# Optimization experiments

Hardware: AMD Instinct MI355X
Metric: run time of the kernel (lower is better)

## Reference

```python
import jax, jax.numpy as jnp
import numpy as np

N_ITER = 2
M = 0.0
AFF_SOFTMAX = 1.0
BIG = 1e16  # finite sentinel for invalid neighbors (CUDA kernel uses inf)


def _ssn(x, s):
    B, C, H, W = x.shape
    nh, nw = H // s, W // s
    S = nh * nw
    N = H * W
    # append_grid: concat (row, col) coordinate channels scaled by M/stoken
    ii, jj = jnp.meshgrid(jnp.arange(H), jnp.arange(W), indexing='ij')
    grid = jnp.stack([ii, jj], 0).astype(x.dtype) * (M / s)  # (2,H,W)
    xg = jnp.concatenate([x, jnp.broadcast_to(grid[None], (B, 2, H, W))], 1)
    C2 = C + 2
    # adaptive_avg_pool2d with exact divisibility == block mean
    cent = xg.reshape(B, C2, nh, s, nw, s).mean(axis=(3, 5)).reshape(B, C2, S)
    # nearest-neighbor init label map (exact divisibility => i//s)
    ly = jnp.broadcast_to((jnp.arange(H) // s)[:, None], (H, W)).reshape(-1)
    lx = jnp.broadcast_to((jnp.arange(W) // s)[None, :], (H, W)).reshape(-1)
    dy = jnp.repeat(jnp.arange(-1, 2), 3)  # 9-neighborhood offsets
    dx = jnp.tile(jnp.arange(-1, 2), 3)
    ny = ly[None, :] + dy[:, None]  # (9,N)
    nx = lx[None, :] + dx[:, None]
    valid = (ny >= 0) & (ny < nh) & (nx >= 0) & (nx < nw)
    nidx = jnp.clip(ny, 0, nh - 1) * nw + jnp.clip(nx, 0, nw - 1)  # (9,N)
    pix = jnp.arange(N)
    bidx = jnp.arange(B)[:, None, None]
    px = xg.reshape(B, C2, N)
    abs_aff = None
    for k in range(N_ITER):
        cg = cent[:, :, nidx]                              # (B,C2,9,N) gather
        dist = ((px[:, :, None, :] - cg) ** 2).sum(1)      # (B,9,N)
        dist = jnp.where(valid[None], dist, BIG)
        aff = jax.nn.softmax(-AFF_SOFTMAX * dist, axis=1)  # softmax over 9 nbrs
        aff = jnp.where(valid[None], aff, 0.0)
        # sparse_coo_tensor(...).to_dense() == scatter-add into (B,S,N)
        abs_aff = jnp.zeros((B, S, N), x.dtype).at[bidx, nidx[None], pix].add(aff)
        if k < N_ITER - 1:
            num = jnp.einsum('bsn,bcn->bcs', abs_aff, px)  # weighted bmm
            den = abs_aff.sum(2)[:, None] + 1e-16
            cent = num / den
    return abs_aff, S


def setup_inputs() -> dict:
    key = jax.random.key(0)
    x = jax.random.normal(key, (4, 32, 256, 256), dtype=jnp.float32)
    return {"x": x, "stoken_size": 16}


def reference(x, stoken_size):
    return _ssn(x, int(stoken_size))
```

## Files before the change

### kernel.cpp

```cpp
#include <hip/hip_runtime.h>
#include <hip/hip_fp16.h>
#include <hip/hip_cooperative_groups.h>

namespace cg = cooperative_groups;

#define B_  4
#define C_  32
#define W_  256
#define N_  65536
#define NH_ 16
#define S_  256
#define PADP 260
#define PADH 260
#define PSTR 304

typedef float vf4 __attribute__((ext_vector_type(4)));
typedef _Float16 h4 __attribute__((ext_vector_type(4)));

__device__ __forceinline__ float wave_sum(float v) {
    v += __shfl_down(v, 32);
    v += __shfl_down(v, 16);
    v += __shfl_down(v, 8);
    v += __shfl_down(v, 4);
    v += __shfl_down(v, 2);
    v += __shfl_down(v, 1);
    return v;
}

__device__ __forceinline__ void st4(float* p, float a, float b, float c, float d) {
    vf4 v = {a, b, c, d};
    *(vf4*)p = v;
}

__device__ __forceinline__ void zero_linear(float* out, int blk, int t,
                                            int i0, int i1) {
    vf4* p = (vf4*)out;
    const size_t base = (size_t)blk * 256 + t;
    const vf4 z = {0.f, 0.f, 0.f, 0.f};
    #pragma unroll 8
    for (int i = i0; i < i1; ++i)
        p[base + (size_t)i * 262144] = z;
}

__device__ __forceinline__ void stage_tile(const float* __restrict__ x,
                                           int b, int sy, int sx, int t,
                                           float (*xsh)[PADP]) {
    const float* base = x + (size_t)b * C_ * N_ + (sy * 16) * W_ + sx * 16;
    #pragma unroll
    for (int i = 0; i < 8; ++i) {
        const int idx = i * 256 + t;
        const int c = idx >> 6, p4 = idx & 63;
        const float4 v = *(const float4*)(base + (size_t)c * N_ + (p4 >> 2) * W_ + (p4 & 3) * 4);
        *(float4*)&xsh[c][p4 * 4] = v;
    }
}

__device__ __forceinline__ void compute_aff(const float xv[C_], const float (*cl)[C_],
                                            int sy, int sx, float aff[9]) {
    float dist[9];
    #pragma unroll
    for (int k = 0; k < 9; ++k) {
        const int ny = sy + k / 3 - 1, nx = sx + k % 3 - 1;
        const bool valid = (ny >= 0) & (ny < NH_) & (nx >= 0) & (nx < NH_);
        float d = 0.f;
        #pragma unroll
        for (int c4 = 0; c4 < C_ / 4; ++c4) {
            const float4 cv = *(const float4*)&cl[k][c4 * 4];
            const float d0 = xv[c4 * 4 + 0] - cv.x;
            const float d1 = xv[c4 * 4 + 1] - cv.y;
            const float d2 = xv[c4 * 4 + 2] - cv.z;
            const float d3 = xv[c4 * 4 + 3] - cv.w;
            d += d0 * d0 + d1 * d1 + d2 * d2 + d3 * d3;
        }
        dist[k] = valid ? d : 1e30f;
    }
    float mind = dist[0];
    #pragma unroll
    for (int k = 1; k < 9; ++k) mind = fminf(mind, dist[k]);
    float sum = 0.f;
    #pragma unroll
    for (int k = 0; k < 9; ++k) {
        const float e = (dist[k] < 1e29f) ? __expf(mind - dist[k]) : 0.f;
        aff[k] = e;
        sum += e;
    }
    const float inv = 1.f / sum;
    #pragma unroll
    for (int k = 0; k < 9; ++k) aff[k] *= inv;
}

__device__ __forceinline__ float gather_cent1(const float* __restrict__ part,
                                              int b, int ny, int nx, int c) {
    float num = 0.f, den = 0.f;
    #pragma unroll
    for (int k2 = 0; k2 < 9; ++k2) {
        const int syp = ny - (k2 / 3 - 1), sxp = nx - (k2 % 3 - 1);
        if ((syp >= 0) & (syp < NH_) & (sxp >= 0) & (sxp < NH_)) {
            const size_t base = (size_t)(b * S_ + syp * NH_ + sxp) * PSTR;
            num += part[base + k2 * 32 + c];
            den += part[base + 288 + k2];
        }
    }
    return num / (den + 1e-16f);
}

__global__ __launch_bounds__(256, 4) void k_fused(const float* __restrict__ x,
                                                  float* __restrict__ cent0,
                                                  float* __restrict__ part,
                                                  float* __restrict__ out) {
    const int blk = blockIdx.x;
    const int b = blk >> 8, s = blk & 255;
    const int sy = s >> 4, sx = s & 15;
    const int t = threadIdx.x;
    const int w = t >> 6, lane = t & 63;
    __shared__ float cl[9][C_];
    __shared__ float xsh[C_][PADP];
    __shared__ _Float16 affs[9][PADH];
    __shared__ float lden[4][9];

    stage_tile(x, b, sy, sx, t, xsh);
    zero_linear(out, blk, t, 0, 32);
    __syncthreads();
    #pragma unroll
    for (int i = 0; i < 8; ++i) {
        const int c = i * 4 + w;
        const float4 v = *(const float4*)&xsh[c][lane * 4];
        const float sm = wave_sum(v.x + v.y + v.z + v.w);
        if (lane == 0) cent0[(size_t)blk * C_ + c] = sm * (1.0f / 256.0f);
    }
    cg::this_grid().sync();

    {
        const int k = t >> 5, c = t & 31;
        const int ny = sy + k / 3 - 1, nx = sx + k % 3 - 1;
        const bool valid = (ny >= 0) & (ny < NH_) & (nx >= 0) & (nx < NH_);
        cl[k][c] = valid ? cent0[(size_t)(b * S_ + ny * NH_ + nx) * C_ + c] : 0.f;
    }
    if (t < 32) {
        const int ny = sy + 1, nx = sx + 1;
        const bool valid = (ny < NH_) & (nx < NH_);
        cl[8][t] = valid ? cent0[(size_t)(b * S_ + ny * NH_ + nx) * C_ + t] : 0.f;
    }
    zero_linear(out, blk, t, 32, 64);
    __syncthreads();
    float xv[C_];
    #pragma unroll
    for (int c = 0; c < C_; ++c) xv[c] = xsh[c][t];
    float aff[9];
    compute_aff(xv, cl, sy, sx, aff);
    #pragma unroll
    for (int k = 0; k < 9; ++k) {
        affs[k][t] = (_Float16)aff[k];
        const float v = wave_sum(aff[k]);
        if (lane == 0) lden[w][k] = v;
    }
    __syncthreads();
    {
        const int k = t >> 5, c = t & 31;
        float acc = 0.f;
        #pragma unroll 4
        for (int p = 0; p < 256; p += 4) {
            const h4 a = *(const h4*)&affs[k][p];
            const float4 xc = *(const float4*)&xsh[c][p];
            acc += (float)a.x * xc.x + (float)a.y * xc.y +
                   (float)a.z * xc.z + (float)a.w * xc.w;
        }
        part[(size_t)blk * PSTR + t] = acc;
    }
    if (t < 32) {
        float acc = 0.f;
        #pragma unroll 4
        for (int p = 0; p < 256; p += 4) {
            const h4 a = *(const h4*)&affs[8][p];
            const float4 xc = *(const float4*)&xsh[t][p];
            acc += (float)a.x * xc.x + (float)a.y * xc.y +
                   (float)a.z * xc.z + (float)a.w * xc.w;
        }
        part[(size_t)blk * PSTR + 256 + t] = acc;
    }
    if (t < 9)
        part[(size_t)blk * PSTR + 288 + t] =
            lden[0][t] + lden[1][t] + lden[2][t] + lden[3][t];
    cg::this_grid().sync();

    {
        const int k = t >> 5, c = t & 31;
        const int ny = sy + k / 3 - 1, nx = sx + k % 3 - 1;
        const bool valid = (ny >= 0) & (ny < NH_) & (nx >= 0) & (nx < NH_);
        cl[k][c] = valid ? gather_cent1(part, b, ny, nx, c) : 0.f;
    }
    if (t < 32) {
        const int ny = sy + 1, nx = sx + 1;
        const bool valid = (ny < NH_) & (nx < NH_);
        cl[8][t] = valid ? gather_cent1(part, b, ny, nx, t) : 0.f;
    }
    __syncthreads();
    #pragma unroll
    for (int c = 0; c < C_; ++c) xv[c] = xsh[c][t];
    compute_aff(xv, cl, sy, sx, aff);
    #pragma unroll
    for (int k = 0; k < 9; ++k) affs[k][t] = (_Float16)aff[k];
    __syncthreads();
    #pragma unroll
    for (int i = 0; i < 3; ++i) {
        const int idx = i * 256 + t;
        if (idx < 576) {
            const int k = idx >> 6, j4 = idx & 63;
            const int ny = sy + k / 3 - 1, nx = sx + k % 3 - 1;
            if ((ny >= 0) & (ny < NH_) & (nx >= 0) & (nx < NH_)) {
                const h4 a = *(const h4*)&affs[k][j4 * 4];
                const int gq = (sy * 16 + (j4 >> 2)) * 64 + sx * 4 + (j4 & 3);
                float* dst = out + (((size_t)(b * S_ + ny * NH_ + nx) << 16) + gq * 4);
                st4(dst, (float)a.x, (float)a.y, (float)a.z, (float)a.w);
            }
        }
    }
    if ((blk | t) == 0) out[(size_t)B_ * S_ * N_] = 256.0f;
}

__global__ __launch_bounds__(256) void k_zero(float* __restrict__ out) {
    const size_t tid = (size_t)blockIdx.x * 256 + threadIdx.x;
    vf4* p = (vf4*)out;
    const vf4 z = {0.f, 0.f, 0.f, 0.f};
    #pragma unroll 4
    for (int i = 0; i < 32; ++i)
        p[tid + (size_t)i * 524288] = z;
}

__global__ __launch_bounds__(256) void k_cent0(const float* __restrict__ x,
                                               float* __restrict__ cent0) {
    const int blk = blockIdx.x;
    const int b = blk >> 8, s = blk & 255;
    const int sy = s >> 4, sx = s & 15;
    const int t = threadIdx.x;
    const int w = t >> 6, lane = t & 63;
    const float* base = x + (size_t)b * C_ * N_ + (sy * 16) * W_ + sx * 16;
    #pragma unroll
    for (int i = 0; i < 8; ++i) {
        const int c = i * 4 + w;
        const float4 v = *(const float4*)(base + (size_t)c * N_ + (lane >> 2) * W_ + (lane & 3) * 4);
        const float sm = wave_sum(v.x + v.y + v.z + v.w);
        if (lane == 0) cent0[(size_t)blk * C_ + c] = sm * (1.0f / 256.0f);
    }
}

__global__ __launch_bounds__(256, 4) void k_part(const float* __restrict__ x,
                                                 const float* __restrict__ cent0,
                                                 float* __restrict__ part) {
    const int blk = blockIdx.x;
    const int b = blk >> 8, s = blk & 255;
    const int sy = s >> 4, sx = s & 15;
    const int t = threadIdx.x;
    const int w = t >> 6, lane = t & 63;
    __shared__ float cl[9][C_];
    __shared__ float xsh[C_][PADP];
    __shared__ _Float16 affs[9][PADH];
    __shared__ float lden[4][9];
    {
        const int k = t >> 5, c = t & 31;
        const int ny = sy + k / 3 - 1, nx = sx + k % 3 - 1;
        const bool valid = (ny >= 0) & (ny < NH_) & (nx >= 0) & (nx < NH_);
        cl[k][c] = valid ? cent0[(size_t)(b * S_ + ny * NH_ + nx) * C_ + c] : 0.f;
    }
    if (t < 32) {
        const int ny = sy + 1, nx = sx + 1;
        const bool valid = (ny < NH_) & (nx < NH_);
        cl[8][t] = valid ? cent0[(size_t)(b * S_ + ny * NH_ + nx) * C_ + t] : 0.f;
    }
    stage_tile(x, b, sy, sx, t, xsh);
    __syncthreads();
    float xv[C_];
    #pragma unroll
    for (int c = 0; c < C_; ++c) xv[c] = xsh[c][t];
    float aff[9];
    compute_aff(xv, cl, sy, sx, aff);
    #pragma unroll
    for (int k = 0; k < 9; ++k) {
        affs[k][t] = (_Float16)aff[k];
        const float v = wave_sum(aff[k]);
        if (lane == 0) lden[w][k] = v;
    }
    __syncthreads();
    {
        const int k = t >> 5, c = t & 31;
        float acc = 0.f;
        #pragma unroll 4
        for (int p = 0; p < 256; p += 4) {
            const h4 a = *(const h4*)&affs[k][p];
            const float4 xc = *(const float4*)&xsh[c][p];
            acc += (float)a.x * xc.x + (float)a.y * xc.y +
                   (float)a.z * xc.z + (float)a.w * xc.w;
        }
        part[(size_t)blk * PSTR + t] = acc;
    }
    if (t < 32) {
        float acc = 0.f;
        #pragma unroll 4
        for (int p = 0; p < 256; p += 4) {
            const h4 a = *(const h4*)&affs[8][p];
            const float4 xc = *(const float4*)&xsh[t][p];
            acc += (float)a.x * xc.x + (float)a.y * xc.y +
                   (float)a.z * xc.z + (float)a.w * xc.w;
        }
        part[(size_t)blk * PSTR + 256 + t] = acc;
    }
    if (t < 9)
        part[(size_t)blk * PSTR + 288 + t] =
            lden[0][t] + lden[1][t] + lden[2][t] + lden[3][t];
}

__global__ __launch_bounds__(256, 4) void k_aff9(const float* __restrict__ x,
                                                 const float* __restrict__ part,
                                                 float* __restrict__ out) {
    const int blk = blockIdx.x;
    const int b = blk >> 8, s = blk & 255;
    const int sy = s >> 4, sx = s & 15;
    const int t = threadIdx.x;
    __shared__ float cl[9][C_];
    __shared__ float xsh[C_][PADP];
    __shared__ _Float16 affs[9][PADH];
    {
        const int k = t >> 5, c = t & 31;
        const int ny = sy + k / 3 - 1, nx = sx + k % 3 - 1;
        const bool valid = (ny >= 0) & (ny < NH_) & (nx >= 0) & (nx < NH_);
        cl[k][c] = valid ? gather_cent1(part, b, ny, nx, c) : 0.f;
    }
    if (t < 32) {
        const int ny = sy + 1, nx = sx + 1;
        const bool valid = (ny < NH_) & (nx < NH_);
        cl[8][t] = valid ? gather_cent1(part, b, ny, nx, t) : 0.f;
    }
    stage_tile(x, b, sy, sx, t, xsh);
    __syncthreads();
    float xv[C_];
    #pragma unroll
    for (int c = 0; c < C_; ++c) xv[c] = xsh[c][t];
    float aff[9];
    compute_aff(xv, cl, sy, sx, aff);
    #pragma unroll
    for (int k = 0; k < 9; ++k) affs[k][t] = (_Float16)aff[k];
    __syncthreads();
    #pragma unroll
    for (int i = 0; i < 3; ++i) {
        const int idx = i * 256 + t;
        if (idx < 576) {
            const int k = idx >> 6, j4 = idx & 63;
            const int ny = sy + k / 3 - 1, nx = sx + k % 3 - 1;
            if ((ny >= 0) & (ny < NH_) & (nx >= 0) & (nx < NH_)) {
                const h4 a = *(const h4*)&affs[k][j4 * 4];
                const int gq = (sy * 16 + (j4 >> 2)) * 64 + sx * 4 + (j4 & 3);
                float* dst = out + (((size_t)(b * S_ + ny * NH_ + nx) << 16) + gq * 4);
                st4(dst, (float)a.x, (float)a.y, (float)a.z, (float)a.w);
            }
        }
    }
    if ((blk | t) == 0) out[(size_t)B_ * S_ * N_] = 256.0f;
}

extern "C" void kernel_launch(void* const* d_in, const int* in_sizes, int n_in,
                              void* d_out, int out_size, void* d_ws, size_t ws_size,
                              hipStream_t stream) {
    const float* x = (const float*)d_in[0];
    float* ws = (float*)d_ws;
    float* cent0 = ws;
    float* part  = ws + 32768;
    float* out   = (float*)d_out;

    static int coop_ok = -1;
    if (coop_ok < 0) {
        int nb = 0;
        hipError_t e = hipOccupancyMaxActiveBlocksPerMultiprocessor(&nb, k_fused, 256, 0);
        coop_ok = (e == hipSuccess && nb >= 4) ? 1 : 0;
    }

    if (coop_ok == 1) {
        void* args[] = {(void*)&x, (void*)&cent0, (void*)&part, (void*)&out};
        hipError_t e = hipLaunchCooperativeKernel((void*)k_fused, dim3(B_ * S_),
                                                  dim3(256), args, 0, stream);
        if (e == hipSuccess) return;
        coop_ok = 0;
    }

    hipLaunchKernelGGL(k_zero,  dim3(2048),    dim3(256), 0, stream, out);
    hipLaunchKernelGGL(k_cent0, dim3(B_ * S_), dim3(256), 0, stream, x, cent0);
    hipLaunchKernelGGL(k_part,  dim3(B_ * S_), dim3(256), 0, stream, x, cent0, part);
    hipLaunchKernelGGL(k_aff9,  dim3(B_ * S_), dim3(256), 0, stream, x, part, out);
}
```

Measured before the change: 348.7 us.

## Write compact affinities to workspace, then emit dense output in one streaming pass

New measurement: 346.2 us. Within noise of the previous version (-0.7%).

```diff
diff --git a/kernel.cpp b/kernel.cpp
--- a/kernel.cpp
+++ b/kernel.cpp
@@ -27,21 +27,6 @@
     return v;
 }
 
-__device__ __forceinline__ void st4(float* p, float a, float b, float c, float d) {
-    vf4 v = {a, b, c, d};
-    *(vf4*)p = v;
-}
-
-__device__ __forceinline__ void zero_linear(float* out, int blk, int t,
-                                            int i0, int i1) {
-    vf4* p = (vf4*)out;
-    const size_t base = (size_t)blk * 256 + t;
-    const vf4 z = {0.f, 0.f, 0.f, 0.f};
-    #pragma unroll 8
-    for (int i = i0; i < i1; ++i)
-        p[base + (size_t)i * 262144] = z;
-}
-
 __device__ __forceinline__ void stage_tile(const float* __restrict__ x,
                                            int b, int sy, int sx, int t,
                                            float (*xsh)[PADP]) {
@@ -104,10 +89,36 @@
     return num / (den + 1e-16f);
 }
 
-__global__ __launch_bounds__(256, 4) void k_fused(const float* __restrict__ x,
-                                                  float* __restrict__ cent0,
-                                                  float* __restrict__ part,
-                                                  float* __restrict__ out) {
+__global__ __launch_bounds__(256) void k_write(const float* __restrict__ vals,
+                                               float* __restrict__ out) {
+    const size_t tid = (size_t)blockIdx.x * 256 + threadIdx.x;
+    vf4* po = (vf4*)out;
+    #pragma unroll 4
+    for (int i = 0; i < 32; ++i) {
+        const size_t q = tid + (size_t)i * 524288;
+        const int b   = (int)(q >> 22);
+        const int r   = (int)(q & 4194303);
+        const int sp  = r >> 14;
+        const int n4  = r & 16383;
+        const int py  = n4 >> 6, px4 = n4 & 63;
+        const int syp = sp >> 4,  sxp = sp & 15;
+        const int ty  = py >> 4,  tx  = px4 >> 2;
+        vf4 v = {0.f, 0.f, 0.f, 0.f};
+        if (((unsigned)(ty - syp + 1) <= 2u) & ((unsigned)(tx - sxp + 1) <= 2u)) {
+            const int ssrc = ty * 16 + tx;
+            const int kp   = (syp - ty + 1) * 3 + (sxp - tx + 1);
+            const int pl   = (py & 15) * 16 + (px4 & 3) * 4;
+            v = *(const vf4*)&vals[(((size_t)(b * S_ + ssrc) * 9) + kp) * 256 + pl];
+        }
+        po[q] = v;
+    }
+    if (tid == 0) out[(size_t)B_ * S_ * N_] = 256.0f;
+}
+
+__global__ __launch_bounds__(256, 4) void k_compute(const float* __restrict__ x,
+                                                    float* __restrict__ cent0,
+                                                    float* __restrict__ part,
+                                                    float* __restrict__ vals) {
     const int blk = blockIdx.x;
     const int b = blk >> 8, s = blk & 255;
     const int sy = s >> 4, sx = s & 15;
@@ -119,7 +130,6 @@
     __shared__ float lden[4][9];
 
     stage_tile(x, b, sy, sx, t, xsh);
-    zero_linear(out, blk, t, 0, 32);
     __syncthreads();
     #pragma unroll
     for (int i = 0; i < 8; ++i) {
@@ -141,7 +151,6 @@
         const bool valid = (ny < NH_) & (nx < NH_);
         cl[8][t] = valid ? cent0[(size_t)(b * S_ + ny * NH_ + nx) * C_ + t] : 0.f;
     }
-    zero_linear(out, blk, t, 32, 64);
     __syncthreads();
     float xv[C_];
     #pragma unroll
@@ -199,32 +208,8 @@
     for (int c = 0; c < C_; ++c) xv[c] = xsh[c][t];
     compute_aff(xv, cl, sy, sx, aff);
     #pragma unroll
-    for (int k = 0; k < 9; ++k) affs[k][t] = (_Float16)aff[k];
-    __syncthreads();
-    #pragma unroll
-    for (int i = 0; i < 3; ++i) {
-        const int idx = i * 256 + t;
-        if (idx < 576) {
-            const int k = idx >> 6, j4 = idx & 63;
-            const int ny = sy + k / 3 - 1, nx = sx + k % 3 - 1;
-            if ((ny >= 0) & (ny < NH_) & (nx >= 0) & (nx < NH_)) {
-                const h4 a = *(const h4*)&affs[k][j4 * 4];
-                const int gq = (sy * 16 + (j4 >> 2)) * 64 + sx * 4 + (j4 & 3);
-                float* dst = out + (((size_t)(b * S_ + ny * NH_ + nx) << 16) + gq * 4);
-                st4(dst, (float)a.x, (float)a.y, (float)a.z, (float)a.w);
-            }
-        }
-    }
-    if ((blk | t) == 0) out[(size_t)B_ * S_ * N_] = 256.0f;
-}
-
-__global__ __launch_bounds__(256) void k_zero(float* __restrict__ out) {
-    const size_t tid = (size_t)blockIdx.x * 256 + threadIdx.x;
-    vf4* p = (vf4*)out;
-    const vf4 z = {0.f, 0.f, 0.f, 0.f};
-    #pragma unroll 4
-    for (int i = 0; i < 32; ++i)
-        p[tid + (size_t)i * 524288] = z;
+    for (int k = 0; k < 9; ++k)
+        vals[(((size_t)blk * 9) + k) * 256 + t] = aff[k];
 }
 
 __global__ __launch_bounds__(256) void k_cent0(const float* __restrict__ x,
@@ -309,16 +294,15 @@
             lden[0][t] + lden[1][t] + lden[2][t] + lden[3][t];
 }
 
-__global__ __launch_bounds__(256, 4) void k_aff9(const float* __restrict__ x,
-                                                 const float* __restrict__ part,
-                                                 float* __restrict__ out) {
+__global__ __launch_bounds__(256, 4) void k_aff9v(const float* __restrict__ x,
+                                                  const float* __restrict__ part,
+                                                  float* __restrict__ vals) {
     const int blk = blockIdx.x;
     const int b = blk >> 8, s = blk & 255;
     const int sy = s >> 4, sx = s & 15;
     const int t = threadIdx.x;
     __shared__ float cl[9][C_];
     __shared__ float xsh[C_][PADP];
-    __shared__ _Float16 affs[9][PADH];
     {
         const int k = t >> 5, c = t & 31;
         const int ny = sy + k / 3 - 1, nx = sx + k % 3 - 1;
@@ -338,23 +322,8 @@
     float aff[9];
     compute_aff(xv, cl, sy, sx, aff);
     #pragma unroll
-    for (int k = 0; k < 9; ++k) affs[k][t] = (_Float16)aff[k];
-    __syncthreads();
-    #pragma unroll
-    for (int i = 0; i < 3; ++i) {
-        const int idx = i * 256 + t;
-        if (idx < 576) {
-            const int k = idx >> 6, j4 = idx & 63;
-            const int ny = sy + k / 3 - 1, nx = sx + k % 3 - 1;
-            if ((ny >= 0) & (ny < NH_) & (nx >= 0) & (nx < NH_)) {
-                const h4 a = *(const h4*)&affs[k][j4 * 4];
-                const int gq = (sy * 16 + (j4 >> 2)) * 64 + sx * 4 + (j4 & 3);
-                float* dst = out + (((size_t)(b * S_ + ny * NH_ + nx) << 16) + gq * 4);
-                st4(dst, (float)a.x, (float)a.y, (float)a.z, (float)a.w);
-            }
-        }
-    }
-    if ((blk | t) == 0) out[(size_t)B_ * S_ * N_] = 256.0f;
+    for (int k = 0; k < 9; ++k)
+        vals[(((size_t)blk * 9) + k) * 256 + t] = aff[k];
 }
 
 extern "C" void kernel_launch(void* const* d_in, const int* in_sizes, int n_in,
@@ -364,25 +333,29 @@
     float* ws = (float*)d_ws;
     float* cent0 = ws;
     float* part  = ws + 32768;
+    float* vals  = ws + 32768 + 311296;
     float* out   = (float*)d_out;
 
     static int coop_ok = -1;
     if (coop_ok < 0) {
         int nb = 0;
-        hipError_t e = hipOccupancyMaxActiveBlocksPerMultiprocessor(&nb, k_fused, 256, 0);
+        hipError_t e = hipOccupancyMaxActiveBlocksPerMultiprocessor(&nb, k_compute, 256, 0);
         coop_ok = (e == hipSuccess && nb >= 4) ? 1 : 0;
     }
 
+    bool launched = false;
     if (coop_ok == 1) {
-        void* args[] = {(void*)&x, (void*)&cent0, (void*)&part, (void*)&out};
-        hipError_t e = hipLaunchCooperativeKernel((void*)k_fused, dim3(B_ * S_),
+        void* args[] = {(void*)&x, (void*)&cent0, (void*)&part, (void*)&vals};
+        hipError_t e = hipLaunchCooperativeKernel((void*)k_compute, dim3(B_ * S_),
                                                   dim3(256), args, 0, stream);
-        if (e == hipSuccess) return;
-        coop_ok = 0;
-    }
-
-    hipLaunchKernelGGL(k_zero,  dim3(2048),    dim3(256), 0, stream, out);
-    hipLaunchKernelGGL(k_cent0, dim3(B_ * S_), dim3(256), 0, stream, x, cent0);
-    hipLaunchKernelGGL(k_part,  dim3(B_ * S_), dim3(256), 0, stream, x, cent0, part);
-    hipLaunchKernelGGL(k_aff9,  dim3(B_ * S_), dim3(256), 0, stream, x, part, out);
-}
+        if (e == hipSuccess) launched = true;
+        else coop_ok = 0;
+    }
+    if (!launched) {
+        hipLaunchKernelGGL(k_cent0, dim3(B_ * S_), dim3(256), 0, stream, x, cent0);
+        hipLaunchKernelGGL(k_part,  dim3(B_ * S_), dim3(256), 0, stream, x, cent0, part);
+        hipLaunchKernelGGL(k_aff9v, dim3(B_ * S_), dim3(256), 0, stream, x, part, vals);
+    }
+
+    hipLaunchKernelGGL(k_write, dim3(2048), dim3(256), 0, stream, vals, out);
+}
```
